# Kernel optimization log

Hardware: AMD Instinct MI355X
Metric: run time of the kernel (lower is better)

The kernel has to match this reference:

```python
import jax, jax.numpy as jnp
import numpy as np

N_ANT = 64      # n_antenna
K = 2           # branching factor
N_BEAM = 64     # n_narrow_beam
N_LAYER = 6     # log_K(N_BEAM); 5 Node layers + 1 Leaf layer
BATCH = 131072


def _dft_codebook():
    # Leaf DFT codebook: steering vectors at azimuths arccos(linspace(cos0, cos(pi-1e-6), N_BEAM))
    az = np.arccos(np.linspace(np.cos(0.0), np.cos(np.pi - 1e-6), N_BEAM))
    A = np.exp(1j * np.pi * np.outer(np.arange(N_ANT), np.cos(az))) / np.sqrt(N_ANT)
    return jnp.asarray(A, dtype=jnp.complex64)  # (N_ANT, N_BEAM)


def setup_inputs() -> dict:
    key = jax.random.key(0)
    keys = jax.random.split(key, N_LAYER)
    inp = {"xbatch": jax.random.normal(keys[0], (BATCH, 2 * N_ANT), dtype=jnp.float32)}
    for l in range(N_LAYER - 1):  # Node layers l=0..4, k^l nodes each, theta (nodes, N_ANT, K)
        inp[f"theta{l}"] = jax.random.normal(keys[l + 1], (K ** l, N_ANT, K), dtype=jnp.float32)
    return inp


def reference(xbatch, theta0, theta1, theta2, theta3, theta4):
    thetas = [theta0, theta1, theta2, theta3, theta4]
    B = xbatch.shape[0]
    # complex channel from stacked [real | imag] input
    h = jax.lax.complex(xbatch[:, :N_ANT], xbatch[:, N_ANT:])  # (B, N_ANT) complex64
    inv_scale = 1.0 / np.sqrt(N_ANT)

    # P holds path probabilities for all nodes at the current depth, flattened.
    P = jnp.ones((B, 1), dtype=xbatch.dtype)
    for theta in thetas:
        # PhaseShifter: W = exp(j*theta)/sqrt(N_ANT), per node  -> (n_nodes, N_ANT, K)
        W = jax.lax.complex(jnp.cos(theta), jnp.sin(theta)) * inv_scale
        y = jnp.einsum('ba,nak->bnk', h, W)          # (B, n_nodes, K) complex
        gain = y.real ** 2 + y.imag ** 2              # ComputePower
        p = jax.nn.softmax(gain, axis=-1)             # per-node softmax over K children
        P = (P[:, :, None] * p).reshape(B, -1)        # extend all tree paths by one layer

    # Leaf layer: fixed DFT codebook, softmax within each group of K narrow beams
    A = _dft_codebook()
    y = (h @ A).reshape(B, N_BEAM // K, K)            # (B, 32, 2) complex
    gain = y.real ** 2 + y.imag ** 2
    p = jax.nn.softmax(gain, axis=-1)
    P = (P[:, :, None] * p).reshape(B, N_BEAM)        # (B, N_BEAM) leaf path probabilities
    return P
```

## Files before the change

### kernel.cpp

```cpp
#include <hip/hip_runtime.h>
#include <math.h>

#define N_ANT 64
#define BATCH 131072
#define NSTEPS 63
#define TPB 1024
#define NBLK 256
#define EPR 32
#define ROUNDS 16
#define PSTR 66

typedef float f32x4 __attribute__((ext_vector_type(4)));
typedef float v2f   __attribute__((ext_vector_type(2)));
typedef _Float16 f16x8 __attribute__((ext_vector_type(8)));
typedef _Float16 f16x4 __attribute__((ext_vector_type(4)));

static __device__ __forceinline__ float fast_rcp(float x) {
#if __has_builtin(__builtin_amdgcn_rcpf)
    return __builtin_amdgcn_rcpf(x);
#else
    return 1.0f / x;
#endif
}

static __device__ __forceinline__ void dfs_next(int& l, int& n) {
    if (l < 5) { l = l + 1; n = 2 * n; }
    else {
        while (n & 1) { n >>= 1; l--; }
        n += 1;
    }
}

__global__ void fill_B(const float* __restrict__ t0, const float* __restrict__ t1,
                       const float* __restrict__ t2, const float* __restrict__ t3,
                       const float* __restrict__ t4,
                       _Float16* __restrict__ B1p, _Float16* __restrict__ B2p) {
    const int t = blockIdx.x * 256 + threadIdx.x;
    const int L = t & 63;
    const int kstep = (t >> 6) & 3;
    const int ntile = t >> 8;
    const int n = ntile * 16 + (L & 15);
    const int kbase = kstep * 32 + (L >> 4) * 8;

    f16x8 h1 = {0,0,0,0,0,0,0,0}, h2 = {0,0,0,0,0,0,0,0};
    if (n < 252) {
        const int c = n >> 1, part = n & 1;
        const int s = c >> 1, kidx = c & 1;
        int l = 0, nn = 0;
        for (int i = 0; i < s; ++i) dfs_next(l, nn);
#pragma unroll
        for (int j = 0; j < 8; ++j) {
            const int k = kbase + j;
            const int a = k & 63;
            const int hi = k >> 6;
            float wr, wi;
            if (l < 5) {
                const float* th = (l == 0) ? t0 : (l == 1) ? t1 : (l == 2) ? t2
                                 : (l == 3) ? t3 : t4;
                float theta = th[(nn * N_ANT + a) * 2 + kidx];
                float sn, cs;
                sincosf(theta, &sn, &cs);
                wr = cs * 0.125f; wi = sn * 0.125f;
            } else {
                const int b = 2 * nn + kidx;
                const double step = (cos(M_PI - 1e-6) - 1.0) / 63.0;
                double cosaz = 1.0 + (double)b * step;
                double ph = M_PI * (double)a * cosaz;
                wr = (float)(cos(ph) * 0.125);
                wi = (float)(sin(ph) * 0.125);
            }
            float v = (part == 0) ? (hi == 0 ? wr : -wi)
                                  : (hi == 0 ? wi :  wr);
            _Float16 v1 = (_Float16)v;
            _Float16 v2 = (_Float16)(v - (float)v1);
            h1[j] = v1; h2[j] = v2;
        }
    }
    *(f16x8*)(B1p + (size_t)t * 8) = h1;
    *(f16x8*)(B2p + (size_t)t * 8) = h2;
}

__global__ __launch_bounds__(TPB) void beam_mfma(const float* __restrict__ x,
                                                 const _Float16* __restrict__ W1p,
                                                 const _Float16* __restrict__ W2p,
                                                 float* __restrict__ out) {
    __shared__ _Float16 xb[2][4096];
    __shared__ float pb[2][64 * PSTR];

    const int tid = threadIdx.x;
    const int w   = tid >> 6;
    const int L   = tid & 63;
    const int q   = L >> 4;
    const int e15 = L & 15;

    f16x8 w1f[4], w2f[4];
#pragma unroll
    for (int ks = 0; ks < 4; ++ks) {
        w1f[ks] = *(const f16x8*)(W1p + (size_t)((w * 4 + ks) * 64 + L) * 8);
        w2f[ks] = *(const f16x8*)(W2p + (size_t)((w * 4 + ks) * 64 + L) * 8);
    }

    int myl = -1, myn = 0;
    {
        int cl = 0, cn = 0;
        for (int s = 0; s < NSTEPS; ++s) {
            if (s == L) { myl = cl; myn = cn; }
            dfs_next(cl, cn);
        }
    }
    const int sd0 = (myn >> 4) & 1, sd1 = (myn >> 3) & 1, sd2 = (myn >> 2) & 1,
              sd3 = (myn >> 1) & 1, sd4 = myn & 1;
    const int a0 = 0;
    const int a1 = a0 + 1 + sd0 * 31;
    const int a2 = a1 + 1 + sd1 * 15;
    const int a3 = a2 + 1 + sd2 * 7;
    const int a4 = a3 + 1 + sd3 * 3;

    const int s_er = tid & 31;
    const int s_rt = tid >> 5;
    const int s_h  = s_rt & 1;
    const int s_q  = (s_rt >> 1) & 3;
    const int s_ks = s_rt >> 3;
    const int s_goff = s_er * 128 + s_ks * 32 + s_q * 8 + s_h * 4;
    const int s_loff = ((s_ks * 4 + s_q) * 32 + s_er) * 8 + s_h * 4;

    const long base = (long)blockIdx.x * (EPR * ROUNDS);

    {
        float4 v = *(const float4*)(x + base * 128 + s_goff);
        f16x4 hv = {(_Float16)v.x, (_Float16)v.y, (_Float16)v.z, (_Float16)v.w};
        *(f16x4*)(&xb[0][s_loff]) = hv;
    }
    __syncthreads();

#pragma unroll 1
    for (int r = 0; r < ROUNDS; ++r) {
        const int cur = r & 1;
        const bool more = (r + 1 < ROUNDS);
        float4 nv = {0.f, 0.f, 0.f, 0.f};
        if (more) nv = *(const float4*)(x + (base + (long)(r + 1) * EPR) * 128 + s_goff);

        f32x4 acc0 = {0,0,0,0}, acc1 = {0,0,0,0};
#pragma unroll
        for (int ks = 0; ks < 4; ++ks) {
            const _Float16* xc = &xb[cur][(size_t)((ks * 4 + q) * 32) * 8];
            f16x8 b0 = *(const f16x8*)(xc + e15 * 8);
            f16x8 b1 = *(const f16x8*)(xc + (16 + e15) * 8);
            acc0 = __builtin_amdgcn_mfma_f32_16x16x32_f16(w1f[ks], b0, acc0, 0, 0, 0);
            acc1 = __builtin_amdgcn_mfma_f32_16x16x32_f16(w1f[ks], b1, acc1, 0, 0, 0);
            acc0 = __builtin_amdgcn_mfma_f32_16x16x32_f16(w2f[ks], b0, acc0, 0, 0, 0);
            acc1 = __builtin_amdgcn_mfma_f32_16x16x32_f16(w2f[ks], b1, acc1, 0, 0, 0);
        }

        if (more) {
            f16x4 hv = {(_Float16)nv.x, (_Float16)nv.y, (_Float16)nv.z, (_Float16)nv.w};
            *(f16x4*)(&xb[cur ^ 1][s_loff]) = hv;
        }

        const int u = 4 * w + q;
#pragma unroll
        for (int g = 0; g < 2; ++g) {
            f32x4 a = g ? acc1 : acc0;
            float g0 = fmaf(a.x, a.x, a.y * a.y);
            float g1 = fmaf(a.z, a.z, a.w * a.w);
            float m  = fmaxf(g0, g1);
            float e0 = __expf(g0 - m);
            float e1 = __expf(g1 - m);
            float inv = fast_rcp(e0 + e1);
            if (u < NSTEPS)
                *(v2f*)(&pb[cur][u * PSTR + 2 * (g * 16 + e15)]) = (v2f){e0 * inv, e1 * inv};
        }
        __syncthreads();

#pragma unroll
        for (int pass = 0; pass < 2; ++pass) {
            const int er = 2 * w + pass;
            v2f pp = *(const v2f*)(&pb[cur][L * PSTR + 2 * er]);
            float p0x = __shfl(pp.x, a0), p0y = __shfl(pp.y, a0);
            float p1x = __shfl(pp.x, a1), p1y = __shfl(pp.y, a1);
            float p2x = __shfl(pp.x, a2), p2y = __shfl(pp.y, a2);
            float p3x = __shfl(pp.x, a3), p3y = __shfl(pp.y, a3);
            float p4x = __shfl(pp.x, a4), p4y = __shfl(pp.y, a4);
            float P = (sd0 ? p0y : p0x) * (sd1 ? p1y : p1x) * (sd2 ? p2y : p2x)
            if (myl == 5) {
                *(v2f*)(out + (base + (long)r * EPR + er) * 64 + 2 * myn) =
                    (v2f){P * pp.x, P * pp.y};
            }
        }
    }
}

extern "C" void kernel_launch(void* const* d_in, const int* in_sizes, int n_in,
                              void* d_out, int out_size, void* d_ws, size_t ws_size,
                              hipStream_t stream) {
    const float* x  = (const float*)d_in[0];
    const float* t0 = (const float*)d_in[1];
    const float* t1 = (const float*)d_in[2];
    const float* t2 = (const float*)d_in[3];
    const float* t3 = (const float*)d_in[4];
    const float* t4 = (const float*)d_in[5];
    _Float16* W1p = (_Float16*)d_ws;
    _Float16* W2p = (_Float16*)((char*)d_ws + 65536);

    fill_B<<<dim3(16), dim3(256), 0, stream>>>(t0, t1, t2, t3, t4, W1p, W2p);
    beam_mfma<<<dim3(NBLK), dim3(TPB), 0, stream>>>(x, W1p, W2p, (float*)d_out);
}
```

Baseline: 142.1 us.

## Fuse weight generation into main kernel and read path probabilities from LDS

Removes the separate fill_B launch: each block now computes its fp16 hi/lo split weight fragments directly from theta (and sincospif for the DFT leaf) in registers. The probability buffer is transposed so each leaf thread reads its ancestor probabilities straight from shared memory instead of through cross-lane shuffles. Grid doubles to 512 blocks with half the rounds each, which adds more redundant per-block weight computation but removes a launch and a global round trip. Per-block setup cost (sincos on 16 elements per thread) grows with block count.

```diff
diff --git a/kernel.cpp b/kernel.cpp
--- a/kernel.cpp
+++ b/kernel.cpp
@@ -5,10 +5,10 @@
 #define BATCH 131072
 #define NSTEPS 63
 #define TPB 1024
-#define NBLK 256
+#define NBLK 512
 #define EPR 32
-#define ROUNDS 16
-#define PSTR 66
+#define ROUNDS 8
+#define PSTR 130
 
 typedef float f32x4 __attribute__((ext_vector_type(4)));
 typedef float v2f   __attribute__((ext_vector_type(2)));
@@ -31,61 +31,15 @@
     }
 }
 
-__global__ void fill_B(const float* __restrict__ t0, const float* __restrict__ t1,
-                       const float* __restrict__ t2, const float* __restrict__ t3,
-                       const float* __restrict__ t4,
-                       _Float16* __restrict__ B1p, _Float16* __restrict__ B2p) {
-    const int t = blockIdx.x * 256 + threadIdx.x;
-    const int L = t & 63;
-    const int kstep = (t >> 6) & 3;
-    const int ntile = t >> 8;
-    const int n = ntile * 16 + (L & 15);
-    const int kbase = kstep * 32 + (L >> 4) * 8;
-
-    f16x8 h1 = {0,0,0,0,0,0,0,0}, h2 = {0,0,0,0,0,0,0,0};
-    if (n < 252) {
-        const int c = n >> 1, part = n & 1;
-        const int s = c >> 1, kidx = c & 1;
-        int l = 0, nn = 0;
-        for (int i = 0; i < s; ++i) dfs_next(l, nn);
-#pragma unroll
-        for (int j = 0; j < 8; ++j) {
-            const int k = kbase + j;
-            const int a = k & 63;
-            const int hi = k >> 6;
-            float wr, wi;
-            if (l < 5) {
-                const float* th = (l == 0) ? t0 : (l == 1) ? t1 : (l == 2) ? t2
-                                 : (l == 3) ? t3 : t4;
-                float theta = th[(nn * N_ANT + a) * 2 + kidx];
-                float sn, cs;
-                sincosf(theta, &sn, &cs);
-                wr = cs * 0.125f; wi = sn * 0.125f;
-            } else {
-                const int b = 2 * nn + kidx;
-                const double step = (cos(M_PI - 1e-6) - 1.0) / 63.0;
-                double cosaz = 1.0 + (double)b * step;
-                double ph = M_PI * (double)a * cosaz;
-                wr = (float)(cos(ph) * 0.125);
-                wi = (float)(sin(ph) * 0.125);
-            }
-            float v = (part == 0) ? (hi == 0 ? wr : -wi)
-                                  : (hi == 0 ? wi :  wr);
-            _Float16 v1 = (_Float16)v;
-            _Float16 v2 = (_Float16)(v - (float)v1);
-            h1[j] = v1; h2[j] = v2;
-        }
-    }
-    *(f16x8*)(B1p + (size_t)t * 8) = h1;
-    *(f16x8*)(B2p + (size_t)t * 8) = h2;
-}
-
 __global__ __launch_bounds__(TPB) void beam_mfma(const float* __restrict__ x,
-                                                 const _Float16* __restrict__ W1p,
-                                                 const _Float16* __restrict__ W2p,
+                                                 const float* __restrict__ t0,
+                                                 const float* __restrict__ t1,
+                                                 const float* __restrict__ t2,
+                                                 const float* __restrict__ t3,
+                                                 const float* __restrict__ t4,
                                                  float* __restrict__ out) {
     __shared__ _Float16 xb[2][4096];
-    __shared__ float pb[2][64 * PSTR];
+    __shared__ float pb[2][EPR * PSTR];
 
     const int tid = threadIdx.x;
     const int w   = tid >> 6;
@@ -96,8 +50,45 @@
     f16x8 w1f[4], w2f[4];
 #pragma unroll
     for (int ks = 0; ks < 4; ++ks) {
-        w1f[ks] = *(const f16x8*)(W1p + (size_t)((w * 4 + ks) * 64 + L) * 8);
-        w2f[ks] = *(const f16x8*)(W2p + (size_t)((w * 4 + ks) * 64 + L) * 8);
+        w1f[ks] = (f16x8){0,0,0,0,0,0,0,0};
+        w2f[ks] = (f16x8){0,0,0,0,0,0,0,0};
+    }
+    {
+        const int m = 16 * w + e15;
+        const int c = m >> 1, part = m & 1;
+        const int su = c >> 1, kidx = c & 1;
+        if (su < NSTEPS) {
+            int l = 0, nn = 0;
+            for (int i = 0; i < su; ++i) dfs_next(l, nn);
+            const float* th = (l == 0) ? t0 : (l == 1) ? t1 : (l == 2) ? t2
+                             : (l == 3) ? t3 : t4;
+            const double step = (cos(M_PI - 1e-6) - 1.0) / 63.0;
+            const double cosaz = 1.0 + (double)(2 * nn + kidx) * step;
+#pragma unroll
+            for (int aidx = 0; aidx < 16; ++aidx) {
+                const int ks = aidx >> 3, j = aidx & 7;
+                const int a = ks * 32 + q * 8 + j;
+                float wr, wi;
+                if (l < 5) {
+                    float theta = th[(nn * N_ANT + a) * 2 + kidx];
+                    float sn, cs;
+                    sincosf(theta, &sn, &cs);
+                    wr = cs * 0.125f; wi = sn * 0.125f;
+                } else {
+                    float tt = (float)((double)a * cosaz);
+                    float sp, cp;
+                    sincospif(tt, &sp, &cp);
+                    wr = cp * 0.125f; wi = sp * 0.125f;
+                }
+                const float vlo = part ? wi : wr;
+                const float vhi = part ? wr : -wi;
+                _Float16 h;
+                h = (_Float16)vlo;
+                w1f[ks][j] = h; w2f[ks][j] = (_Float16)(vlo - (float)h);
+                h = (_Float16)vhi;
+                w1f[ks + 2][j] = h; w2f[ks + 2][j] = (_Float16)(vhi - (float)h);
+            }
+        }
     }
 
     int myl = -1, myn = 0;
@@ -168,23 +159,27 @@
             float e1 = __expf(g1 - m);
             float inv = fast_rcp(e0 + e1);
             if (u < NSTEPS)
-                *(v2f*)(&pb[cur][u * PSTR + 2 * (g * 16 + e15)]) = (v2f){e0 * inv, e1 * inv};
+                *(v2f*)(&pb[cur][(g * 16 + e15) * PSTR + 2 * u]) =
+                    (v2f){e0 * inv, e1 * inv};
         }
         __syncthreads();
 
 #pragma unroll
         for (int pass = 0; pass < 2; ++pass) {
             const int er = 2 * w + pass;
-            v2f pp = *(const v2f*)(&pb[cur][L * PSTR + 2 * er]);
-            float p0x = __shfl(pp.x, a0), p0y = __shfl(pp.y, a0);
-            float p1x = __shfl(pp.x, a1), p1y = __shfl(pp.y, a1);
-            float p2x = __shfl(pp.x, a2), p2y = __shfl(pp.y, a2);
-            float p3x = __shfl(pp.x, a3), p3y = __shfl(pp.y, a3);
-            float p4x = __shfl(pp.x, a4), p4y = __shfl(pp.y, a4);
-            float P = (sd0 ? p0y : p0x) * (sd1 ? p1y : p1x) * (sd2 ? p2y : p2x)
+            const float* prow = &pb[cur][er * PSTR];
             if (myl == 5) {
+                v2f own = *(const v2f*)(prow + 2 * L);
+                v2f q0 = *(const v2f*)(prow + 2 * a0);
+                v2f q1 = *(const v2f*)(prow + 2 * a1);
+                v2f q2 = *(const v2f*)(prow + 2 * a2);
+                v2f q3 = *(const v2f*)(prow + 2 * a3);
+                v2f q4 = *(const v2f*)(prow + 2 * a4);
+                float P = (sd0 ? q0.y : q0.x) * (sd1 ? q1.y : q1.x)
+                        * (sd2 ? q2.y : q2.x) * (sd3 ? q3.y : q3.x)
+                        * (sd4 ? q4.y : q4.x);
                 *(v2f*)(out + (base + (long)r * EPR + er) * 64 + 2 * myn) =
-                    (v2f){P * pp.x, P * pp.y};
+                    (v2f){P * own.x, P * own.y};
             }
         }
     }
@@ -199,9 +194,6 @@
     const float* t2 = (const float*)d_in[3];
     const float* t3 = (const float*)d_in[4];
     const float* t4 = (const float*)d_in[5];
-    _Float16* W1p = (_Float16*)d_ws;
-    _Float16* W2p = (_Float16*)((char*)d_ws + 65536);
-
-    fill_B<<<dim3(16), dim3(256), 0, stream>>>(t0, t1, t2, t3, t4, W1p, W2p);
-    beam_mfma<<<dim3(NBLK), dim3(TPB), 0, stream>>>(x, W1p, W2p, (float*)d_out);
+    beam_mfma<<<dim3(NBLK), dim3(TPB), 0, stream>>>(x, t0, t1, t2, t3, t4,
+                                                    (float*)d_out);
 }
```

New measurement: 152.8 us. 7.5% more time.

## Software-pipeline tree product behind next round's MFMAs and double grid size

Applied to the files above, without the earlier changes.

Moves the per-leaf path-product pass one round later so it overlaps the next round's MFMA work. This removes one barrier-bound phase from the critical path of each round. It also transposes the probability buffer so leaf threads read ancestor probabilities directly from LDS instead of using cross-lane shuffles. It splits the hi/lo fp16 MFMA accumulators into independent chains to shorten dependency stalls. Blocks are doubled and rounds halved for more parallelism, at the cost of fewer rounds per block to amortise weight-fragment loads and the prologue.

```diff
diff --git a/kernel.cpp b/kernel.cpp
--- a/kernel.cpp
+++ b/kernel.cpp
@@ -5,10 +5,10 @@
 #define BATCH 131072
 #define NSTEPS 63
 #define TPB 1024
-#define NBLK 256
+#define NBLK 512
 #define EPR 32
-#define ROUNDS 16
-#define PSTR 66
+#define ROUNDS 8
+#define PSTR 130
 
 typedef float f32x4 __attribute__((ext_vector_type(4)));
 typedef float v2f   __attribute__((ext_vector_type(2)));
@@ -85,7 +85,7 @@
                                                  const _Float16* __restrict__ W2p,
                                                  float* __restrict__ out) {
     __shared__ _Float16 xb[2][4096];
-    __shared__ float pb[2][64 * PSTR];
+    __shared__ float pb[2][EPR * PSTR];
 
     const int tid = threadIdx.x;
     const int w   = tid >> 6;
@@ -126,6 +126,27 @@
 
     const long base = (long)blockIdx.x * (EPR * ROUNDS);
 
+    auto tree_pass = [&](int bb, int rr) {
+#pragma unroll
+        for (int pass = 0; pass < 2; ++pass) {
+            const int er = 2 * w + pass;
+            const float* prow = &pb[bb][er * PSTR];
+            if (myl == 5) {
+                v2f own = *(const v2f*)(prow + 2 * L);
+                v2f q0 = *(const v2f*)(prow + 2 * a0);
+                v2f q1 = *(const v2f*)(prow + 2 * a1);
+                v2f q2 = *(const v2f*)(prow + 2 * a2);
+                v2f q3 = *(const v2f*)(prow + 2 * a3);
+                v2f q4 = *(const v2f*)(prow + 2 * a4);
+                float P = (sd0 ? q0.y : q0.x) * (sd1 ? q1.y : q1.x)
+                        * (sd2 ? q2.y : q2.x) * (sd3 ? q3.y : q3.x)
+                        * (sd4 ? q4.y : q4.x);
+                *(v2f*)(out + (base + (long)rr * EPR + er) * 64 + 2 * myn) =
+                    (v2f){P * own.x, P * own.y};
+            }
+        }
+    };
+
     {
         float4 v = *(const float4*)(x + base * 128 + s_goff);
         f16x4 hv = {(_Float16)v.x, (_Float16)v.y, (_Float16)v.z, (_Float16)v.w};
@@ -140,27 +161,27 @@
         float4 nv = {0.f, 0.f, 0.f, 0.f};
         if (more) nv = *(const float4*)(x + (base + (long)(r + 1) * EPR) * 128 + s_goff);
 
-        f32x4 acc0 = {0,0,0,0}, acc1 = {0,0,0,0};
+        f32x4 acc0a = {0,0,0,0}, acc0b = {0,0,0,0};
+        f32x4 acc1a = {0,0,0,0}, acc1b = {0,0,0,0};
 #pragma unroll
         for (int ks = 0; ks < 4; ++ks) {
             const _Float16* xc = &xb[cur][(size_t)((ks * 4 + q) * 32) * 8];
             f16x8 b0 = *(const f16x8*)(xc + e15 * 8);
             f16x8 b1 = *(const f16x8*)(xc + (16 + e15) * 8);
-            acc0 = __builtin_amdgcn_mfma_f32_16x16x32_f16(w1f[ks], b0, acc0, 0, 0, 0);
-            acc1 = __builtin_amdgcn_mfma_f32_16x16x32_f16(w1f[ks], b1, acc1, 0, 0, 0);
-            acc0 = __builtin_amdgcn_mfma_f32_16x16x32_f16(w2f[ks], b0, acc0, 0, 0, 0);
-            acc1 = __builtin_amdgcn_mfma_f32_16x16x32_f16(w2f[ks], b1, acc1, 0, 0, 0);
-        }
-
-        if (more) {
-            f16x4 hv = {(_Float16)nv.x, (_Float16)nv.y, (_Float16)nv.z, (_Float16)nv.w};
-            *(f16x4*)(&xb[cur ^ 1][s_loff]) = hv;
-        }
+            acc0a = __builtin_amdgcn_mfma_f32_16x16x32_f16(w1f[ks], b0, acc0a, 0, 0, 0);
+            acc1a = __builtin_amdgcn_mfma_f32_16x16x32_f16(w1f[ks], b1, acc1a, 0, 0, 0);
+            acc0b = __builtin_amdgcn_mfma_f32_16x16x32_f16(w2f[ks], b0, acc0b, 0, 0, 0);
+            acc1b = __builtin_amdgcn_mfma_f32_16x16x32_f16(w2f[ks], b1, acc1b, 0, 0, 0);
+        }
+
+        if (r > 0) tree_pass(cur ^ 1, r - 1);
 
         const int u = 4 * w + q;
+        f32x4 A0 = acc0a + acc0b;
+        f32x4 A1 = acc1a + acc1b;
 #pragma unroll
         for (int g = 0; g < 2; ++g) {
-            f32x4 a = g ? acc1 : acc0;
+            f32x4 a = g ? A1 : A0;
             float g0 = fmaf(a.x, a.x, a.y * a.y);
             float g1 = fmaf(a.z, a.z, a.w * a.w);
             float m  = fmaxf(g0, g1);
@@ -168,26 +189,18 @@
             float e1 = __expf(g1 - m);
             float inv = fast_rcp(e0 + e1);
             if (u < NSTEPS)
-                *(v2f*)(&pb[cur][u * PSTR + 2 * (g * 16 + e15)]) = (v2f){e0 * inv, e1 * inv};
+                *(v2f*)(&pb[cur][(g * 16 + e15) * PSTR + 2 * u]) =
+                    (v2f){e0 * inv, e1 * inv};
+        }
+
+        if (more) {
+            f16x4 hv = {(_Float16)nv.x, (_Float16)nv.y, (_Float16)nv.z, (_Float16)nv.w};
+            *(f16x4*)(&xb[cur ^ 1][s_loff]) = hv;
         }
         __syncthreads();
-
-#pragma unroll
-        for (int pass = 0; pass < 2; ++pass) {
-            const int er = 2 * w + pass;
-            v2f pp = *(const v2f*)(&pb[cur][L * PSTR + 2 * er]);
-            float p0x = __shfl(pp.x, a0), p0y = __shfl(pp.y, a0);
-            float p1x = __shfl(pp.x, a1), p1y = __shfl(pp.y, a1);
-            float p2x = __shfl(pp.x, a2), p2y = __shfl(pp.y, a2);
-            float p3x = __shfl(pp.x, a3), p3y = __shfl(pp.y, a3);
-            float p4x = __shfl(pp.x, a4), p4y = __shfl(pp.y, a4);
-            float P = (sd0 ? p0y : p0x) * (sd1 ? p1y : p1x) * (sd2 ? p2y : p2x)
-            if (myl == 5) {
-                *(v2f*)(out + (base + (long)r * EPR + er) * 64 + 2 * myn) =
-                    (v2f){P * pp.x, P * pp.y};
-            }
-        }
-    }
+    }
+
+    tree_pass((ROUNDS - 1) & 1, ROUNDS - 1);
 }
 
 extern "C" void kernel_launch(void* const* d_in, const int* in_sizes, int n_in,
```

Measured after the change: 147.1 us. +3.5%, slower.
